# Kernel tuning notes

Measured on AMD Instinct MI355X. Metric: run time of the kernel, lower is better.

The kernel has to match this reference:

```python
import jax, jax.numpy as jnp
import numpy as np

B, V, NB, K = 4, 5023, 10, 9
# (Cin, Cout) per NLayer: encoder Linear(3->16) then 3 encoder NLayers, 3 decoder NLayers, Linear(3->3)
CH = [(16, 16), (16, 16), (16, 32), (32, 16), (16, 16), (16, 3)]


def _glorot(key, shape):
    fan_in, fan_out = shape[0], shape[-1]
    s = np.float32(np.sqrt(2.0 / (fan_in + fan_out)))
    return (jax.random.normal(key, shape, dtype=jnp.float32) * s)


def setup_inputs():
    key = jax.random.key(0)
    ks = jax.random.split(key, 4 + 4 * len(CH))
    inp = {}
    inp["x"] = jax.random.normal(ks[0], (B, V, 3), dtype=jnp.float32)
    inp["adj"] = jax.random.randint(ks[1], (V, NB), 0, V + 1, dtype=jnp.int32)
    inp["Win"] = _glorot(ks[2], (3, CH[0][0]))
    inp["Wout"] = _glorot(ks[3], (CH[-1][1], 3))
    for i, (cin, cout) in enumerate(CH):
        k0, k1, k2, k3 = ks[4 + 4 * i], ks[5 + 4 * i], ks[6 + 4 * i], ks[7 + 4 * i]
        inp[f"W{i}"] = _glorot(k0, (cin, K, cout))
        inp[f"b{i}"] = jax.random.normal(k1, (cout,), dtype=jnp.float32) * 0.01
        inp[f"u{i}"] = _glorot(k2, (cin, K))
        inp[f"c{i}"] = jax.random.normal(k3, (K,), dtype=jnp.float32) * 0.01
    return inp


def _pad_gather(t, adj):
    # t: [B, V, ...]; pad a zero row at vertex index 0, gather neighbor features.
    z = jnp.zeros(t.shape[:1] + (1,) + t.shape[2:], t.dtype)
    return jnp.take(jnp.concatenate([z, t], axis=1), adj, axis=1)  # [B, V, NB, ...]


def _nlayer(h, adj, recip, W, b, u, c):
    # h: [B, V, Cin], W: [Cin, K, Cout], u: [Cin, K]
    wx = jnp.einsum('bvc,cko->bvko', h, W)          # [B, V, K, Cout]
    nb_w = _pad_gather(wx, adj)                      # [B, V, NB, K, Cout]
    ux = jnp.einsum('bvc,ck->bvk', h, u)             # [B, V, K]  (u and v maps share self.u)
    nb_u = _pad_gather(ux, adj)                      # [B, V, NB, K]
    q = jax.nn.softmax(ux[:, :, None, :] + nb_u + c, axis=-1)  # softmax over kernel dim
    out = jnp.einsum('bvnk,bvnko->bvo', q, nb_w)     # sum over neighbors & kernels
    return out * recip[None, :, None] + b


def reference(x, adj, Win, Wout, W0, b0, u0, c0, W1, b1, u1, c1, W2, b2, u2, c2,
              W3, b3, u3, c3, W4, b4, u4, c4, W5, b5, u5, c5):
    cnt = jnp.sum(adj != 0, axis=-1).astype(jnp.float32)        # [V]
    recip = jnp.where(cnt > 0, 1.0 / jnp.maximum(cnt, 1.0), 0.0)
    h = jax.nn.relu(x @ Win)
    layers = [(W0, b0, u0, c0), (W1, b1, u1, c1), (W2, b2, u2, c2),
              (W3, b3, u3, c3), (W4, b4, u4, c4), (W5, b5, u5, c5)]
    for (W, b, u, c) in layers:
        h = jax.nn.relu(_nlayer(h, adj, recip, W, b, u, c))
    return h @ Wout
```

## Files before the change

### kernel.cpp

```cpp
#include <hip/hip_runtime.h>

#define NBK 10
#define KK  9

constexpr int Bv  = 4;
constexpr int Vv  = 5023;
constexpr int TOT = Bv * Vv;


__device__ __forceinline__ float merge16(float* a, int t)
{
#pragma unroll
    for (int j = 0; j < 8; j++) {
        float send = (t & 8) ? a[j] : a[j + 8];
        float keep = (t & 8) ? a[j + 8] : a[j];
        a[j] = keep + __shfl_xor(send, 8, 16);
    }
#pragma unroll
    for (int j = 0; j < 4; j++) {
        float send = (t & 4) ? a[j] : a[j + 4];
        float keep = (t & 4) ? a[j + 4] : a[j];
        a[j] = keep + __shfl_xor(send, 4, 16);
    }
#pragma unroll
    for (int j = 0; j < 2; j++) {
        float send = (t & 2) ? a[j] : a[j + 2];
        float keep = (t & 2) ? a[j + 2] : a[j];
        a[j] = keep + __shfl_xor(send, 2, 16);
    }
    {
        float send = (t & 1) ? a[0] : a[1];
        float keep = (t & 1) ? a[1] : a[0];
        a[0] = keep + __shfl_xor(send, 1, 16);
    }
    return a[0];
}

__global__ __launch_bounds__(256, 4) void enc_l0_kernel(
    const float* __restrict__ x, const int* __restrict__ adj,
    const float* __restrict__ Win, const float* __restrict__ u0,
    const float* __restrict__ W, const float* __restrict__ bvec,
    const float* __restrict__ cvec, const float* __restrict__ unx,
    float* __restrict__ hux_out)
{
    constexpr int COUTP = 20;
    __shared__ __align__(16) float s_w[KK * 16 * COUTP];

    const int tid = threadIdx.x;

    {
        constexpr int NF4 = 16 * KK * 16 / 4;
        constexpr int KC4 = KK * 16 / 4;
        const float4* W4 = reinterpret_cast<const float4*>(W);
        for (int i = tid; i < NF4; i += 256) {
            const int c   = i / KC4;
            const int rem = i - c * KC4;
            const int k   = rem >> 2;
            const int o4  = rem & 3;
            *reinterpret_cast<float4*>(&s_w[(k * 16 + c) * COUTP + o4 * 4]) = W4[i];
        }
    }
    __syncthreads();

    const int g = tid >> 4;
    const int t = tid & 15;
    const int vv = blockIdx.x * 16 + g;
    if (vv >= TOT) return;
    const int b = vv / Vv;
    const int v = vv - b * Vv;
    const float* xB = x + (size_t)b * Vv * 3;

    int nb[NBK];
    const int2* arow = reinterpret_cast<const int2*>(&adj[v * NBK]);
#pragma unroll
    for (int j = 0; j < 5; j++) { int2 p = arow[j]; nb[2 * j] = p.x; nb[2 * j + 1] = p.y; }
    int cnt = 0;
#pragma unroll
    for (int n = 0; n < NBK; n++) cnt += (nb[n] != 0) ? 1 : 0;
    const float rec = cnt ? (1.0f / (float)cnt) : 0.0f;

    const float w0 = Win[t], w1 = Win[16 + t], w2 = Win[32 + t];
    float hn0[NBK];
#pragma unroll
    for (int n = 0; n < NBK; n++) {
        const int a = nb[n];
        float x0 = 0.f, x1 = 0.f, x2 = 0.f;
        if (a) {
            const float* xr = &xB[(size_t)(a - 1) * 3];
            x0 = xr[0]; x1 = xr[1]; x2 = xr[2];
        }
        hn0[n] = fmaxf(x0 * w0 + x1 * w1 + x2 * w2, 0.0f);
    }

    float q[KK] = {};
    if (t < NBK) {
        const float* xo = &xB[(size_t)v * 3];
        const float xo0 = xo[0], xo1 = xo[1], xo2 = xo[2];
        const int a = nb[t];
        float xn0 = 0.f, xn1 = 0.f, xn2 = 0.f;
        if (a) {
            const float* xr = &xB[(size_t)(a - 1) * 3];
            xn0 = xr[0]; xn1 = xr[1]; xn2 = xr[2];
        }
        float hs[16];
#pragma unroll
        for (int c = 0; c < 16; c++) {
            const float ho = fmaxf(xo0 * Win[c] + xo1 * Win[16 + c] + xo2 * Win[32 + c], 0.0f);
            const float hn = fmaxf(xn0 * Win[c] + xn1 * Win[16 + c] + xn2 * Win[32 + c], 0.0f);
            hs[c] = ho + hn;
        }
        float lg[KK];
#pragma unroll
        for (int k = 0; k < KK; k++) {
            float s = cvec[k];
#pragma unroll
            for (int c = 0; c < 16; c++) s = fmaf(hs[c], u0[c * KK + k], s);
            lg[k] = s;
        }
        float m = lg[0];
#pragma unroll
        for (int k = 1; k < KK; k++) m = fmaxf(m, lg[k]);
        float sum = 0.0f;
#pragma unroll
        for (int k = 0; k < KK; k++) { q[k] = __expf(lg[k] - m); sum += q[k]; }
        const float r = 1.0f / sum;
#pragma unroll
        for (int k = 0; k < KK; k++) q[k] *= r;
    }

    float g0[KK];
#pragma unroll
    for (int k = 0; k < KK; k++) g0[k] = 0.0f;
#pragma unroll
    for (int n = 0; n < NBK; n++) {
#pragma unroll
        for (int k = 0; k < KK; k++) {
            const float qnk = __shfl(q[k], n, 16);
            g0[k] = fmaf(qnk, hn0[n], g0[k]);
        }
    }

    float acc[16] = {};
#pragma unroll
    for (int k = 0; k < KK; k++) {
        const float g0k = g0[k];
        const float* wr = &s_w[(k * 16 + t) * COUTP];
#pragma unroll
        for (int o4 = 0; o4 < 4; o4++) {
            const float4 w = *reinterpret_cast<const float4*>(&wr[4 * o4]);
            acc[4 * o4 + 0] = fmaf(g0k, w.x, acc[4 * o4 + 0]);
            acc[4 * o4 + 1] = fmaf(g0k, w.y, acc[4 * o4 + 1]);
            acc[4 * o4 + 2] = fmaf(g0k, w.z, acc[4 * o4 + 2]);
            acc[4 * o4 + 3] = fmaf(g0k, w.w, acc[4 * o4 + 3]);
        }
    }

    const float o0 = merge16(acc, t);
    const float h0v = fmaxf(fmaf(o0, rec, bvec[t]), 0.0f);
    float* row = &hux_out[(size_t)vv * 32];
    row[t] = h0v;

    float uxv = 0.0f;
#pragma unroll
    for (int o = 0; o < 16; o++) {
        const float hb = __shfl(h0v, o, 16);
        if (t < KK) uxv = fmaf(hb, unx[o * KK + t], uxv);
    }
    if (t < KK) row[16 + t] = uxv;
}

template<int CIN, int COUT, bool LAST, int RSI, int RSO>
__global__ __launch_bounds__(512, 4) void nlayer_kernel(
    const float* __restrict__ hux_in,
    const int*   __restrict__ adj,
    const float* __restrict__ W,
    const float* __restrict__ bvec,
    const float* __restrict__ cvec,
    const float* __restrict__ unx,
    float* __restrict__ hux_out,
    float* __restrict__ dout)
{
    constexpr int COUTP = (COUT == 32) ? 36 : ((COUT == 16) ? 20 : 4);

    __shared__ __align__(16) float s_w[KK * CIN * COUTP];
    __shared__ __align__(16) float s_q[32][NBK][12];

    const int tid = threadIdx.x;
    const int g = tid >> 4;
    const int t = tid & 15;
    const int vv = blockIdx.x * 32 + g;
    const bool act = vv < TOT;
    int b = 0, v = 0;
    if (act) { b = vv / Vv; v = vv - b * Vv; }
    const float* inB = hux_in + (size_t)b * Vv * RSI;

    int nb[NBK];
    if (act) {
        const int2* arow = reinterpret_cast<const int2*>(&adj[v * NBK]);
#pragma unroll
        for (int j = 0; j < 5; j++) { int2 p = arow[j]; nb[2 * j] = p.x; nb[2 * j + 1] = p.y; }
    } else {
#pragma unroll
        for (int n = 0; n < NBK; n++) nb[n] = 0;
    }
    int cnt = 0;
#pragma unroll
    for (int n = 0; n < NBK; n++) cnt += (nb[n] != 0) ? 1 : 0;
    const float rec = cnt ? (1.0f / (float)cnt) : 0.0f;

    float hn0[NBK], hn1[NBK];
#pragma unroll
    for (int n = 0; n < NBK; n++) {
        const int a = nb[n];
        const float* r = &inB[(size_t)(a - 1) * RSI];
        hn0[n] = a ? r[t] : 0.0f;
        if constexpr (CIN == 32) hn1[n] = a ? r[t + 16] : 0.0f;
        else                     hn1[n] = 0.0f;
    }

    float4 s0 = make_float4(0.f, 0.f, 0.f, 0.f), s1 = s0, n0 = s0, n1 = s0;
    float  s8 = 0.f, n8 = 0.f;
    if (t < NBK) {
        const float* su = &inB[(size_t)v * RSI + CIN];
        s0 = *reinterpret_cast<const float4*>(su);
        s1 = *reinterpret_cast<const float4*>(su + 4);
        s8 = su[8];
        const int a = nb[t];
        if (a) {
            const float* nu = &inB[(size_t)(a - 1) * RSI + CIN];
            n0 = *reinterpret_cast<const float4*>(nu);
            n1 = *reinterpret_cast<const float4*>(nu + 4);
            n8 = nu[8];
        }
    }

    if constexpr (!LAST) {
        constexpr int NF4 = CIN * KK * COUT / 4;
        constexpr int KC4 = KK * COUT / 4;
        constexpr int C4  = COUT / 4;
        const float4* W4 = reinterpret_cast<const float4*>(W);
        for (int i = tid; i < NF4; i += 512) {
            const int c   = i / KC4;
            const int rem = i - c * KC4;
            const int k   = rem / C4;
            const int o4  = rem - k * C4;
            *reinterpret_cast<float4*>(&s_w[(k * CIN + c) * COUTP + o4 * 4]) = W4[i];
        }
    } else {
        for (int i = tid; i < CIN * KK * 3; i += 512) {
            const int c   = i / (KK * 3);
            const int rem = i - c * (KK * 3);
            const int k   = rem / 3;
            const int o   = rem - k * 3;
            s_w[(k * CIN + c) * COUTP + o] = W[i];
        }
    }
    __syncthreads();
    if (!act) return;

    if (t < NBK) {
        float lg[KK] = { s0.x + n0.x + cvec[0], s0.y + n0.y + cvec[1],
                         s0.z + n0.z + cvec[2], s0.w + n0.w + cvec[3],
                         s1.x + n1.x + cvec[4], s1.y + n1.y + cvec[5],
                         s1.z + n1.z + cvec[6], s1.w + n1.w + cvec[7],
                         s8 + n8 + cvec[8] };
        float m = lg[0];
#pragma unroll
        for (int k = 1; k < KK; k++) m = fmaxf(m, lg[k]);
        float e[KK], sum = 0.0f;
#pragma unroll
        for (int k = 0; k < KK; k++) { e[k] = __expf(lg[k] - m); sum += e[k]; }
        const float r = 1.0f / sum;
        *reinterpret_cast<float4*>(&s_q[g][t][0]) =
            make_float4(e[0] * r, e[1] * r, e[2] * r, e[3] * r);
        *reinterpret_cast<float4*>(&s_q[g][t][4]) =
            make_float4(e[4] * r, e[5] * r, e[6] * r, e[7] * r);
        s_q[g][t][8] = e[8] * r;
    }

    float g0[KK], g1[KK];
#pragma unroll
    for (int k = 0; k < KK; k++) { g0[k] = 0.0f; g1[k] = 0.0f; }
#pragma unroll
    for (int n = 0; n < NBK; n++) {
        const float4 qa = *reinterpret_cast<const float4*>(&s_q[g][n][0]);
        const float4 qb = *reinterpret_cast<const float4*>(&s_q[g][n][4]);
        const float  q8 = s_q[g][n][8];
        const float h0 = hn0[n];
        g0[0] = fmaf(qa.x, h0, g0[0]); g0[1] = fmaf(qa.y, h0, g0[1]);
        g0[2] = fmaf(qa.z, h0, g0[2]); g0[3] = fmaf(qa.w, h0, g0[3]);
        g0[4] = fmaf(qb.x, h0, g0[4]); g0[5] = fmaf(qb.y, h0, g0[5]);
        g0[6] = fmaf(qb.z, h0, g0[6]); g0[7] = fmaf(qb.w, h0, g0[7]);
        g0[8] = fmaf(q8,   h0, g0[8]);
        if constexpr (CIN == 32) {
            const float h1 = hn1[n];
            g1[0] = fmaf(qa.x, h1, g1[0]); g1[1] = fmaf(qa.y, h1, g1[1]);
            g1[2] = fmaf(qa.z, h1, g1[2]); g1[3] = fmaf(qa.w, h1, g1[3]);
            g1[4] = fmaf(qb.x, h1, g1[4]); g1[5] = fmaf(qb.y, h1, g1[5]);
            g1[6] = fmaf(qb.z, h1, g1[6]); g1[7] = fmaf(qb.w, h1, g1[7]);
            g1[8] = fmaf(q8,   h1, g1[8]);
        }
    }

    if constexpr (!LAST) {
        float acc[COUT] = {};
#pragma unroll
        for (int k = 0; k < KK; k++) {
            const float g0k = g0[k];
            const float* wr = &s_w[(k * CIN + t) * COUTP];
#pragma unroll
            for (int o4 = 0; o4 < COUT / 4; o4++) {
                const float4 w = *reinterpret_cast<const float4*>(&wr[4 * o4]);
                acc[4 * o4 + 0] = fmaf(g0k, w.x, acc[4 * o4 + 0]);
                acc[4 * o4 + 1] = fmaf(g0k, w.y, acc[4 * o4 + 1]);
                acc[4 * o4 + 2] = fmaf(g0k, w.z, acc[4 * o4 + 2]);
                acc[4 * o4 + 3] = fmaf(g0k, w.w, acc[4 * o4 + 3]);
            }
            if constexpr (CIN == 32) {
                const float g1k = g1[k];
                const float* wr2 = &s_w[(k * CIN + t + 16) * COUTP];
#pragma unroll
                for (int o4 = 0; o4 < COUT / 4; o4++) {
                    const float4 w = *reinterpret_cast<const float4*>(&wr2[4 * o4]);
                    acc[4 * o4 + 0] = fmaf(g1k, w.x, acc[4 * o4 + 0]);
                    acc[4 * o4 + 1] = fmaf(g1k, w.y, acc[4 * o4 + 1]);
                    acc[4 * o4 + 2] = fmaf(g1k, w.z, acc[4 * o4 + 2]);
                    acc[4 * o4 + 3] = fmaf(g1k, w.w, acc[4 * o4 + 3]);
                }
            }
        }

        const float o0 = merge16(acc, t);
        const float h0v = fmaxf(fmaf(o0, rec, bvec[t]), 0.0f);
        float* row = &hux_out[(size_t)vv * RSO];
        row[t] = h0v;
        float h1v = 0.0f;
        if constexpr (COUT == 32) {
            const float o1 = merge16(acc + 16, t);
            h1v = fmaxf(fmaf(o1, rec, bvec[t + 16]), 0.0f);
            row[16 + t] = h1v;
        }

        float uxv = 0.0f;
#pragma unroll
        for (int o = 0; o < 16; o++) {
            const float hb = __shfl(h0v, o, 16);
            if (t < KK) uxv = fmaf(hb, unx[o * KK + t], uxv);
        }
        if constexpr (COUT == 32) {
#pragma unroll
            for (int o = 0; o < 16; o++) {
                const float hb = __shfl(h1v, o, 16);
                if (t < KK) uxv = fmaf(hb, unx[(o + 16) * KK + t], uxv);
            }
        }
        if (t < KK) row[COUT + t] = uxv;
    } else {
        float acc[3] = {};
#pragma unroll
        for (int k = 0; k < KK; k++) {
            const float4 w = *reinterpret_cast<const float4*>(&s_w[(k * CIN + t) * COUTP]);
            acc[0] = fmaf(g0[k], w.x, acc[0]);
            acc[1] = fmaf(g0[k], w.y, acc[1]);
            acc[2] = fmaf(g0[k], w.z, acc[2]);
        }
#pragma unroll
        for (int o = 0; o < 3; o++) {
            acc[o] += __shfl_xor(acc[o], 1, 16);
            acc[o] += __shfl_xor(acc[o], 2, 16);
            acc[o] += __shfl_xor(acc[o], 4, 16);
            acc[o] += __shfl_xor(acc[o], 8, 16);
        }
        float hnew[3];
#pragma unroll
        for (int o = 0; o < 3; o++)
            hnew[o] = fmaxf(fmaf(acc[o], rec, bvec[o]), 0.0f);
        if (t < 3) {
            float s = 0.0f;
#pragma unroll
            for (int j = 0; j < 3; j++)
                s = fmaf(hnew[j], unx[j * 3 + t], s);
            dout[(size_t)vv * 3 + t] = s;
        }
    }
}

extern "C" void kernel_launch(void* const* d_in, const int* in_sizes, int n_in,
                              void* d_out, int out_size, void* d_ws, size_t ws_size,
                              hipStream_t stream)
{
    const float* x    = (const float*)d_in[0];
    const int*   adj  = (const int*)  d_in[1];
    const float* Win  = (const float*)d_in[2];
    const float* Wout = (const float*)d_in[3];
    const float *W[6], *bb[6], *uu[6], *cc[6];
    for (int i = 0; i < 6; i++) {
        W[i]  = (const float*)d_in[4 + 4 * i];
        bb[i] = (const float*)d_in[5 + 4 * i];
        uu[i] = (const float*)d_in[6 + 4 * i];
        cc[i] = (const float*)d_in[7 + 4 * i];
    }
    float* out = (float*)d_out;

    float* p  = (float*)d_ws;
    float* B1 = p; p += (size_t)TOT * 32;
    float* B2 = p; p += (size_t)TOT * 32;
    float* B3 = p; p += (size_t)TOT * 48;
    float* B4 = p; p += (size_t)TOT * 32;
    float* B5 = p; p += (size_t)TOT * 32;

    const int nb1 = (TOT + 15) / 16;
    const int nb2 = (TOT + 31) / 32;

    enc_l0_kernel<<<nb1, 256, 0, stream>>>(x, adj, Win, uu[0], W[0], bb[0], cc[0],
                                           uu[1], B1);
    nlayer_kernel<16, 16, false, 32, 32><<<nb2, 512, 0, stream>>>(B1, adj, W[1], bb[1], cc[1], uu[2], B2, nullptr);
    nlayer_kernel<16, 32, false, 32, 48><<<nb2, 512, 0, stream>>>(B2, adj, W[2], bb[2], cc[2], uu[3], B3, nullptr);
    nlayer_kernel<32, 16, false, 48, 32><<<nb2, 512, 0, stream>>>(B3, adj, W[3], bb[3], cc[3], uu[4], B4, nullptr);
    nlayer_kernel<16, 16, false, 32, 32><<<nb2, 512, 0, stream>>>(B4, adj, W[4], bb[4], cc[4], uu[5], B5, nullptr);
    nlayer_kernel<16, 3, true, 32, 32><<<nb2, 512, 0, stream>>>(B5, adj, W[5], bb[5], cc[5], Wout, nullptr, out);
}
```

Baseline: 78.47 us.

## Fuse all six layers into one persistent kernel with grid-wide atomic barriers

```diff
diff --git a/kernel.cpp b/kernel.cpp
--- a/kernel.cpp
+++ b/kernel.cpp
@@ -2,11 +2,45 @@
 
 #define NBK 10
 #define KK  9
+#define SC_AGENT __HIP_MEMORY_SCOPE_AGENT
 
 constexpr int Bv  = 4;
 constexpr int Vv  = 5023;
 constexpr int TOT = Bv * Vv;
-
+constexpr int NBLK_F = 1256;
+constexpr int NBARS  = 5;
+
+
+struct Bar {
+    int lo[16 * 32];
+    int hi;   int p1[31];
+    int flag; int p2[31];
+};
+
+__device__ __forceinline__ void bar_sync(Bar* bar, int bid, int tid)
+{
+    __syncthreads();
+    if (tid == 0) {
+        const int g    = bid & 15;
+        const int need = (NBLK_F >> 4) + ((g < (NBLK_F & 15)) ? 1 : 0);
+        const int old = __hip_atomic_fetch_add(&bar->lo[g * 32], 1,
+                                               __ATOMIC_RELAXED, SC_AGENT);
+        if (old == need - 1) {
+            const int oh = __hip_atomic_fetch_add(&bar->hi, 1,
+                                                  __ATOMIC_RELAXED, SC_AGENT);
+            if (oh == 15)
+                __hip_atomic_store(&bar->flag, 1, __ATOMIC_RELAXED, SC_AGENT);
+        }
+        while (__hip_atomic_load(&bar->flag, __ATOMIC_RELAXED, SC_AGENT) == 0)
+            __builtin_amdgcn_s_sleep(2);
+    }
+    __syncthreads();
+}
+
+__device__ __forceinline__ void sto(float* p, float v)
+{
+    __hip_atomic_store(p, v, __ATOMIC_RELAXED, SC_AGENT);
+}
 
 __device__ __forceinline__ float merge16(float* a, int t)
 {
@@ -36,18 +70,17 @@
     return a[0];
 }
 
-__global__ __launch_bounds__(256, 4) void enc_l0_kernel(
-    const float* __restrict__ x, const int* __restrict__ adj,
-    const float* __restrict__ Win, const float* __restrict__ u0,
-    const float* __restrict__ W, const float* __restrict__ bvec,
-    const float* __restrict__ cvec, const float* __restrict__ unx,
-    float* __restrict__ hux_out)
+template<bool STO>
+__device__ __forceinline__ void layer0_body(
+    int tid, int g, int t, bool act, int b, int v, int vv,
+    const int* nb, float rec,
+    const float* __restrict__ x, const float* __restrict__ Win,
+    const float* __restrict__ u0, const float* __restrict__ W,
+    const float* __restrict__ bvec, const float* __restrict__ cvec,
+    const float* __restrict__ unx, float* __restrict__ hux_out,
+    float* s_w)
 {
     constexpr int COUTP = 20;
-    __shared__ __align__(16) float s_w[KK * 16 * COUTP];
-
-    const int tid = threadIdx.x;
-
     {
         constexpr int NF4 = 16 * KK * 16 / 4;
         constexpr int KC4 = KK * 16 / 4;
@@ -62,28 +95,12 @@
     }
     __syncthreads();
 
-    const int g = tid >> 4;
-    const int t = tid & 15;
-    const int vv = blockIdx.x * 16 + g;
-    if (vv >= TOT) return;
-    const int b = vv / Vv;
-    const int v = vv - b * Vv;
     const float* xB = x + (size_t)b * Vv * 3;
-
-    int nb[NBK];
-    const int2* arow = reinterpret_cast<const int2*>(&adj[v * NBK]);
-#pragma unroll
-    for (int j = 0; j < 5; j++) { int2 p = arow[j]; nb[2 * j] = p.x; nb[2 * j + 1] = p.y; }
-    int cnt = 0;
-#pragma unroll
-    for (int n = 0; n < NBK; n++) cnt += (nb[n] != 0) ? 1 : 0;
-    const float rec = cnt ? (1.0f / (float)cnt) : 0.0f;
-
     const float w0 = Win[t], w1 = Win[16 + t], w2 = Win[32 + t];
     float hn0[NBK];
 #pragma unroll
     for (int n = 0; n < NBK; n++) {
-        const int a = nb[n];
+        const int a = act ? nb[n] : 0;
         float x0 = 0.f, x1 = 0.f, x2 = 0.f;
         if (a) {
             const float* xr = &xB[(size_t)(a - 1) * 3];
@@ -93,7 +110,7 @@
     }
 
     float q[KK] = {};
-    if (t < NBK) {
+    if (act && t < NBK) {
         const float* xo = &xB[(size_t)v * 3];
         const float xo0 = xo[0], xo1 = xo[1], xo2 = xo[2];
         const int a = nb[t];
@@ -157,8 +174,10 @@
 
     const float o0 = merge16(acc, t);
     const float h0v = fmaxf(fmaf(o0, rec, bvec[t]), 0.0f);
-    float* row = &hux_out[(size_t)vv * 32];
-    row[t] = h0v;
+    if (act) {
+        if (STO) sto(&hux_out[(size_t)vv * 32 + t], h0v);
+        else     hux_out[(size_t)vv * 32 + t] = h0v;
+    }
 
     float uxv = 0.0f;
 #pragma unroll
@@ -166,52 +185,29 @@
         const float hb = __shfl(h0v, o, 16);
         if (t < KK) uxv = fmaf(hb, unx[o * KK + t], uxv);
     }
-    if (t < KK) row[16 + t] = uxv;
-}
-
-template<int CIN, int COUT, bool LAST, int RSI, int RSO>
-__global__ __launch_bounds__(512, 4) void nlayer_kernel(
+    if (act && t < KK) {
+        if (STO) sto(&hux_out[(size_t)vv * 32 + 16 + t], uxv);
+        else     hux_out[(size_t)vv * 32 + 16 + t] = uxv;
+    }
+}
+
+template<int CIN, int COUT, bool LAST, int RSI, int RSO, bool STO, int NSTRIDE>
+__device__ __forceinline__ void nlayer_body(
+    int tid, int g, int t, bool act, int b, int v, int vv,
+    const int* nb, float rec,
     const float* __restrict__ hux_in,
-    const int*   __restrict__ adj,
-    const float* __restrict__ W,
-    const float* __restrict__ bvec,
-    const float* __restrict__ cvec,
-    const float* __restrict__ unx,
-    float* __restrict__ hux_out,
-    float* __restrict__ dout)
+    const float* __restrict__ W, const float* __restrict__ bvec,
+    const float* __restrict__ cvec, const float* __restrict__ unx,
+    float* __restrict__ hux_out, float* __restrict__ dout,
+    float* s_w, float (*s_q)[NBK][12])
 {
     constexpr int COUTP = (COUT == 32) ? 36 : ((COUT == 16) ? 20 : 4);
-
-    __shared__ __align__(16) float s_w[KK * CIN * COUTP];
-    __shared__ __align__(16) float s_q[32][NBK][12];
-
-    const int tid = threadIdx.x;
-    const int g = tid >> 4;
-    const int t = tid & 15;
-    const int vv = blockIdx.x * 32 + g;
-    const bool act = vv < TOT;
-    int b = 0, v = 0;
-    if (act) { b = vv / Vv; v = vv - b * Vv; }
     const float* inB = hux_in + (size_t)b * Vv * RSI;
 
-    int nb[NBK];
-    if (act) {
-        const int2* arow = reinterpret_cast<const int2*>(&adj[v * NBK]);
-#pragma unroll
-        for (int j = 0; j < 5; j++) { int2 p = arow[j]; nb[2 * j] = p.x; nb[2 * j + 1] = p.y; }
-    } else {
-#pragma unroll
-        for (int n = 0; n < NBK; n++) nb[n] = 0;
-    }
-    int cnt = 0;
-#pragma unroll
-    for (int n = 0; n < NBK; n++) cnt += (nb[n] != 0) ? 1 : 0;
-    const float rec = cnt ? (1.0f / (float)cnt) : 0.0f;
-
     float hn0[NBK], hn1[NBK];
 #pragma unroll
     for (int n = 0; n < NBK; n++) {
-        const int a = nb[n];
+        const int a = act ? nb[n] : 0;
         const float* r = &inB[(size_t)(a - 1) * RSI];
         hn0[n] = a ? r[t] : 0.0f;
         if constexpr (CIN == 32) hn1[n] = a ? r[t + 16] : 0.0f;
@@ -220,7 +216,7 @@
 
     float4 s0 = make_float4(0.f, 0.f, 0.f, 0.f), s1 = s0, n0 = s0, n1 = s0;
     float  s8 = 0.f, n8 = 0.f;
-    if (t < NBK) {
+    if (act && t < NBK) {
         const float* su = &inB[(size_t)v * RSI + CIN];
         s0 = *reinterpret_cast<const float4*>(su);
         s1 = *reinterpret_cast<const float4*>(su + 4);
@@ -239,7 +235,7 @@
         constexpr int KC4 = KK * COUT / 4;
         constexpr int C4  = COUT / 4;
         const float4* W4 = reinterpret_cast<const float4*>(W);
-        for (int i = tid; i < NF4; i += 512) {
+        for (int i = tid; i < NF4; i += NSTRIDE) {
             const int c   = i / KC4;
             const int rem = i - c * KC4;
             const int k   = rem / C4;
@@ -247,7 +243,7 @@
             *reinterpret_cast<float4*>(&s_w[(k * CIN + c) * COUTP + o4 * 4]) = W4[i];
         }
     } else {
-        for (int i = tid; i < CIN * KK * 3; i += 512) {
+        for (int i = tid; i < CIN * KK * 3; i += NSTRIDE) {
             const int c   = i / (KK * 3);
             const int rem = i - c * (KK * 3);
             const int k   = rem / 3;
@@ -256,9 +252,8 @@
         }
     }
     __syncthreads();
-    if (!act) return;
-
-    if (t < NBK) {
+
+    if (act && t < NBK) {
         float lg[KK] = { s0.x + n0.x + cvec[0], s0.y + n0.y + cvec[1],
                          s0.z + n0.z + cvec[2], s0.w + n0.w + cvec[3],
                          s1.x + n1.x + cvec[4], s1.y + n1.y + cvec[5],
@@ -333,12 +328,12 @@
         const float o0 = merge16(acc, t);
         const float h0v = fmaxf(fmaf(o0, rec, bvec[t]), 0.0f);
         float* row = &hux_out[(size_t)vv * RSO];
-        row[t] = h0v;
+        if (act) { if (STO) sto(&row[t], h0v); else row[t] = h0v; }
         float h1v = 0.0f;
         if constexpr (COUT == 32) {
             const float o1 = merge16(acc + 16, t);
             h1v = fmaxf(fmaf(o1, rec, bvec[t + 16]), 0.0f);
-            row[16 + t] = h1v;
+            if (act) { if (STO) sto(&row[16 + t], h1v); else row[16 + t] = h1v; }
         }
 
         float uxv = 0.0f;
@@ -354,7 +349,10 @@
                 if (t < KK) uxv = fmaf(hb, unx[(o + 16) * KK + t], uxv);
             }
         }
-        if (t < KK) row[COUT + t] = uxv;
+        if (act && t < KK) {
+            if (STO) sto(&row[COUT + t], uxv);
+            else     row[COUT + t] = uxv;
+        }
     } else {
         float acc[3] = {};
 #pragma unroll
@@ -375,7 +373,7 @@
 #pragma unroll
         for (int o = 0; o < 3; o++)
             hnew[o] = fmaxf(fmaf(acc[o], rec, bvec[o]), 0.0f);
-        if (t < 3) {
+        if (act && t < 3) {
             float s = 0.0f;
 #pragma unroll
             for (int j = 0; j < 3; j++)
@@ -383,6 +381,128 @@
             dout[(size_t)vv * 3 + t] = s;
         }
     }
+}
+
+struct KArgs {
+    const float* x; const int* adj; const float* Win; const float* Wout;
+    const float* W[6]; const float* bv[6]; const float* uv[6]; const float* cv[6];
+    Bar* bars;
+    float* B1; float* B2; float* B3; float* B4; float* B5;
+    float* out;
+};
+
+__global__ __launch_bounds__(256, 5) void fused_kernel(KArgs A)
+{
+    __shared__ __align__(16) float s_w[5760];
+    __shared__ __align__(16) float s_q[16][NBK][12];
+
+    const int tid = threadIdx.x;
+    const int bid = blockIdx.x;
+    const int g = tid >> 4;
+    const int t = tid & 15;
+    const int vv = bid * 16 + g;
+    const bool act = vv < TOT;
+    int b = 0, v = 0;
+    if (act) { b = vv / Vv; v = vv - b * Vv; }
+
+    int nb[NBK];
+    if (act) {
+        const int2* arow = reinterpret_cast<const int2*>(&A.adj[v * NBK]);
+#pragma unroll
+        for (int j = 0; j < 5; j++) { int2 p = arow[j]; nb[2 * j] = p.x; nb[2 * j + 1] = p.y; }
+    } else {
+#pragma unroll
+        for (int n = 0; n < NBK; n++) nb[n] = 0;
+    }
+    int cnt = 0;
+#pragma unroll
+    for (int n = 0; n < NBK; n++) cnt += (nb[n] != 0) ? 1 : 0;
+    const float rec = cnt ? (1.0f / (float)cnt) : 0.0f;
+
+    layer0_body<true>(tid, g, t, act, b, v, vv, nb, rec,
+        A.x, A.Win, A.uv[0], A.W[0], A.bv[0], A.cv[0], A.uv[1], A.B1, s_w);
+    bar_sync(&A.bars[0], bid, tid);
+    nlayer_body<16, 16, false, 32, 32, true, 256>(tid, g, t, act, b, v, vv, nb, rec,
+        A.B1, A.W[1], A.bv[1], A.cv[1], A.uv[2], A.B2, nullptr, s_w, s_q);
+    bar_sync(&A.bars[1], bid, tid);
+    nlayer_body<16, 32, false, 32, 48, true, 256>(tid, g, t, act, b, v, vv, nb, rec,
+        A.B2, A.W[2], A.bv[2], A.cv[2], A.uv[3], A.B3, nullptr, s_w, s_q);
+    bar_sync(&A.bars[2], bid, tid);
+    nlayer_body<32, 16, false, 48, 32, true, 256>(tid, g, t, act, b, v, vv, nb, rec,
+        A.B3, A.W[3], A.bv[3], A.cv[3], A.uv[4], A.B4, nullptr, s_w, s_q);
+    bar_sync(&A.bars[3], bid, tid);
+    nlayer_body<16, 16, false, 32, 32, true, 256>(tid, g, t, act, b, v, vv, nb, rec,
+        A.B4, A.W[4], A.bv[4], A.cv[4], A.uv[5], A.B5, nullptr, s_w, s_q);
+    bar_sync(&A.bars[4], bid, tid);
+    nlayer_body<16, 3, true, 32, 32, true, 256>(tid, g, t, act, b, v, vv, nb, rec,
+        A.B5, A.W[5], A.bv[5], A.cv[5], A.Wout, nullptr, A.out, s_w, s_q);
+}
+
+__global__ __launch_bounds__(256, 4) void enc_l0_kernel(
+    const float* __restrict__ x, const int* __restrict__ adj,
+    const float* __restrict__ Win, const float* __restrict__ u0,
+    const float* __restrict__ W, const float* __restrict__ bvec,
+    const float* __restrict__ cvec, const float* __restrict__ unx,
+    float* __restrict__ hux_out)
+{
+    __shared__ __align__(16) float s_w[KK * 16 * 20];
+    const int tid = threadIdx.x;
+    const int g = tid >> 4;
+    const int t = tid & 15;
+    const int vv = blockIdx.x * 16 + g;
+    const bool act = vv < TOT;
+    int b = 0, v = 0;
+    if (act) { b = vv / Vv; v = vv - b * Vv; }
+    int nb[NBK];
+    if (act) {
+        const int2* arow = reinterpret_cast<const int2*>(&adj[v * NBK]);
+#pragma unroll
+        for (int j = 0; j < 5; j++) { int2 p = arow[j]; nb[2 * j] = p.x; nb[2 * j + 1] = p.y; }
+    } else {
+#pragma unroll
+        for (int n = 0; n < NBK; n++) nb[n] = 0;
+    }
+    int cnt = 0;
+#pragma unroll
+    for (int n = 0; n < NBK; n++) cnt += (nb[n] != 0) ? 1 : 0;
+    const float rec = cnt ? (1.0f / (float)cnt) : 0.0f;
+    layer0_body<false>(tid, g, t, act, b, v, vv, nb, rec,
+        x, Win, u0, W, bvec, cvec, unx, hux_out, s_w);
+}
+
+template<int CIN, int COUT, bool LAST, int RSI, int RSO>
+__global__ __launch_bounds__(512, 4) void nlayer_kernel(
+    const float* __restrict__ hux_in, const int* __restrict__ adj,
+    const float* __restrict__ W, const float* __restrict__ bvec,
+    const float* __restrict__ cvec, const float* __restrict__ unx,
+    float* __restrict__ hux_out, float* __restrict__ dout)
+{
+    constexpr int COUTP = (COUT == 32) ? 36 : ((COUT == 16) ? 20 : 4);
+    __shared__ __align__(16) float s_w[KK * CIN * COUTP];
+    __shared__ __align__(16) float s_q[32][NBK][12];
+    const int tid = threadIdx.x;
+    const int g = tid >> 4;
+    const int t = tid & 15;
+    const int vv = blockIdx.x * 32 + g;
+    const bool act = vv < TOT;
+    int b = 0, v = 0;
+    if (act) { b = vv / Vv; v = vv - b * Vv; }
+    int nb[NBK];
+    if (act) {
+        const int2* arow = reinterpret_cast<const int2*>(&adj[v * NBK]);
+#pragma unroll
+        for (int j = 0; j < 5; j++) { int2 p = arow[j]; nb[2 * j] = p.x; nb[2 * j + 1] = p.y; }
+    } else {
+#pragma unroll
+        for (int n = 0; n < NBK; n++) nb[n] = 0;
+    }
+    int cnt = 0;
+#pragma unroll
+    for (int n = 0; n < NBK; n++) cnt += (nb[n] != 0) ? 1 : 0;
+    const float rec = cnt ? (1.0f / (float)cnt) : 0.0f;
+    nlayer_body<CIN, COUT, LAST, RSI, RSO, false, 512>(tid, g, t, act, b, v, vv, nb, rec,
+        hux_in, W, bvec, cvec, unx, hux_out, dout, s_w,
+        reinterpret_cast<float(*)[NBK][12]>(s_q));
 }
 
 extern "C" void kernel_launch(void* const* d_in, const int* in_sizes, int n_in,
@@ -402,16 +522,36 @@
     }
     float* out = (float*)d_out;
 
-    float* p  = (float*)d_ws;
+    char*  wsb  = (char*)d_ws;
+    Bar*   bars = (Bar*)wsb;
+    float* p    = (float*)(wsb + 16384);
     float* B1 = p; p += (size_t)TOT * 32;
     float* B2 = p; p += (size_t)TOT * 32;
     float* B3 = p; p += (size_t)TOT * 48;
     float* B4 = p; p += (size_t)TOT * 32;
     float* B5 = p; p += (size_t)TOT * 32;
 
+    int dev = 0, ncu = 0, maxb = 0;
+    (void)hipGetDevice(&dev);
+    (void)hipDeviceGetAttribute(&ncu, hipDeviceAttributeMultiprocessorCount, dev);
+    hipError_t oe = hipOccupancyMaxActiveBlocksPerMultiprocessor(&maxb, fused_kernel, 256, 0);
+    const bool use_fused = (oe == hipSuccess) && (ncu > 0) &&
+                           ((long)maxb * ncu >= NBLK_F);
+
+    if (use_fused) {
+        (void)hipMemsetAsync(d_ws, 0, sizeof(Bar) * NBARS, stream);
+        KArgs A;
+        A.x = x; A.adj = adj; A.Win = Win; A.Wout = Wout;
+        for (int i = 0; i < 6; i++) { A.W[i] = W[i]; A.bv[i] = bb[i]; A.uv[i] = uu[i]; A.cv[i] = cc[i]; }
+        A.bars = bars;
+        A.B1 = B1; A.B2 = B2; A.B3 = B3; A.B4 = B4; A.B5 = B5;
+        A.out = out;
+        fused_kernel<<<NBLK_F, 256, 0, stream>>>(A);
+        return;
+    }
+
     const int nb1 = (TOT + 15) / 16;
     const int nb2 = (TOT + 31) / 32;
-
     enc_l0_kernel<<<nb1, 256, 0, stream>>>(x, adj, Win, uu[0], W[0], bb[0], cc[0],
                                            uu[1], B1);
     nlayer_kernel<16, 16, false, 32, 32><<<nb2, 512, 0, stream>>>(B1, adj, W[1], bb[1], cc[1], uu[2], B2, nullptr);
```

Result: slower. 111.1 us (+41.6%).
